# Kernel optimization log

Measured on AMD Instinct MI355X. Metric: run time of the kernel, lower is better.

Reference implementation:

```python
import jax, jax.numpy as jnp
import numpy as np
import math

WS = 8           # window size
NUM_HEADS = 8
LN_EPS = 1e-5


def window_partition(x, ws):
    # x: [B, H, W, C] -> [B*nH*nW, ws, ws, C]
    B, H, W, C = x.shape
    x = x.reshape(B, H // ws, ws, W // ws, ws, C)
    return x.transpose(0, 1, 3, 2, 4, 5).reshape(-1, ws, ws, C)


def window_reverse(w, ws, H, W):
    # w: [B*nH*nW, ws, ws, C] -> [B, H, W, C]
    B = w.shape[0] // ((H // ws) * (W // ws))
    x = w.reshape(B, H // ws, W // ws, ws, ws, -1)
    return x.transpose(0, 1, 3, 2, 4, 5).reshape(B, H, W, -1)


def layernorm(x, g, b):
    mu = jnp.mean(x, axis=-1, keepdims=True)
    var = jnp.mean(jnp.square(x - mu), axis=-1, keepdims=True)
    return (x - mu) * jax.lax.rsqrt(var + LN_EPS) * g + b


def rotation_grid(H, W, ws):
    """Vectorized rotation_process lookup table -> sampling grid [H, W, 2]=(lat,lon)."""
    nH, nW = H // ws, W // ws
    r = 1.0 / ws
    seq = -1.0 + r + 2.0 * r * jnp.arange(ws, dtype=jnp.float32)  # make_coord centers
    ch, cw = jnp.meshgrid(seq, seq, indexing='ij')
    t0 = ch.reshape(-1) / nH                       # [ws*ws] latitude template
    t1 = cw.reshape(-1) / nW                       # [ws*ws] longitude template
    beta = (2.0 * (jnp.arange(nH, dtype=jnp.float32) + 0.5) / nH - 1.0) * (math.pi / 2)  # [nH]
    th = t0 * (math.pi / 2) + math.pi / 2
    ph = t1 * math.pi
    sb, cb = jnp.sin(beta)[:, None], jnp.cos(beta)[:, None]
    st, ct = jnp.sin(th)[None, :], jnp.cos(th)[None, :]
    sp, cp = jnp.sin(ph)[None, :], jnp.cos(ph)[None, :]
    new_th = jnp.arccos(-sb * st * cp + cb * ct)                    # [nH, ws*ws]
    new_ph = jnp.arctan2(st * sp, cb * st * cp + sb * ct)
    lat = jnp.clip((new_th - math.pi / 2) / (math.pi / 2), -1.0, 1.0)
    lon = new_ph / math.pi
    shift = 2.0 * (0.5 - (jnp.arange(nW, dtype=jnp.float32) + 0.5) / nW)
    lon = lon[:, None, :] - shift[None, :, None]                    # [nH, nW, ws*ws]
    lon = jnp.where(lon > 1.0, lon - 2.0, lon)
    lon = jnp.where(lon < -1.0, lon + 2.0, lon)
    lat = jnp.broadcast_to(lat[:, None, :], lon.shape)
    g = jnp.stack([lat, lon], axis=-1).reshape(nH, nW, ws, ws, 2)
    return g.transpose(0, 2, 1, 3, 4).reshape(H, W, 2)


def grid_sample_nearest(im, grid):
    """F.grid_sample(mode='nearest', align_corners=False, padding='zeros').
    im: [B, H, W, C]; grid: [H, W, 2]=(y,x) normalized; shared across batch."""
    B, H, W, C = im.shape
    gy, gx = grid[..., 0], grid[..., 1]
    iy = jnp.round(((gy + 1.0) * H - 1.0) / 2.0).astype(jnp.int32)
    ix = jnp.round(((gx + 1.0) * W - 1.0) / 2.0).astype(jnp.int32)
    valid = (iy >= 0) & (iy < H) & (ix >= 0) & (ix < W)
    iyc = jnp.clip(iy, 0, H - 1)
    ixc = jnp.clip(ix, 0, W - 1)
    out = im[:, iyc, ixc, :]                                        # [B, H, W, C]
    return out * valid[None, :, :, None].astype(im.dtype)


def dwconv3x3(x, w, b):
    # x: [B, C, H, W], w: [C, 1, 3, 3] depthwise
    y = jax.lax.conv_general_dilated(x, w, (1, 1), 'SAME',
                                     feature_group_count=x.shape[1],
                                     dimension_numbers=('NCHW', 'OIHW', 'NCHW'))
    return y + b[None, :, None, None]


def setup_inputs() -> dict:
    key = jax.random.key(0)
    B, H, W, C, dff = 8, 64, 128, 256, 1024
    ks = jax.random.split(key, 10)
    s = 0.02
    return {
        'x': jax.random.normal(ks[0], (B, H * W, C), jnp.float32),
        'H': H, 'W': W,
        'norm1_g': jnp.ones((C,), jnp.float32),
        'norm1_b': jnp.zeros((C,), jnp.float32),
        'wq': jax.random.normal(ks[1], (C, C), jnp.float32) * s,
        'bq': jnp.zeros((C,), jnp.float32),
        'wk': jax.random.normal(ks[2], (C, C), jnp.float32) * s,
        'bk': jnp.zeros((C,), jnp.float32),
        'wv': jax.random.normal(ks[3], (C, C), jnp.float32) * s,
        'bv': jnp.zeros((C,), jnp.float32),
        'rpe_w': jax.random.normal(ks[4], (C, 1, 3, 3), jnp.float32) * s,
        'rpe_b': jnp.zeros((C,), jnp.float32),
        'proj_w': jax.random.normal(ks[5], (C, C), jnp.float32) * s,
        'proj_b': jnp.zeros((C,), jnp.float32),
        'norm2_g': jnp.ones((C,), jnp.float32),
        'norm2_b': jnp.zeros((C,), jnp.float32),
        'fc1_w': jax.random.normal(ks[6], (C, dff), jnp.float32) * s,
        'fc1_b': jnp.zeros((dff,), jnp.float32),
        'fc2_w': jax.random.normal(ks[7], (dff, C), jnp.float32) * s,
        'fc2_b': jnp.zeros((C,), jnp.float32),
    }


def reference(x, H, W, norm1_g, norm1_b, wq, bq, wk, bk, wv, bv, rpe_w, rpe_b,
              proj_w, proj_b, norm2_g, norm2_b, fc1_w, fc1_b, fc2_w, fc2_b):
    B, L, C = x.shape
    ws, nh = WS, NUM_HEADS
    hd = C // nh
    scale = hd ** (-0.5)
    N = ws * ws

    shortcut = x
    xn = layernorm(x, norm1_g, norm1_b).reshape(B, H, W, C)
    # panoramic rotation of the key features (rotation_process)
    y = grid_sample_nearest(xn, rotation_grid(H, W, ws))

    xw = window_partition(xn, ws).reshape(-1, N, C)   # [Bw, N, C]
    yw = window_partition(y, ws).reshape(-1, N, C)
    Bw = xw.shape[0]

    q = xw @ wq + bq
    # depthwise-conv positional term on window-reversed q (rpe_table)
    qimg = window_reverse(q.reshape(-1, ws, ws, C), ws, H, W).transpose(0, 3, 1, 2)  # [B,C,H,W]
    lepe = window_partition(dwconv3x3(qimg, rpe_w, rpe_b).transpose(0, 2, 3, 1), ws).reshape(-1, N, C)

    k = yw @ wk + bk
    v = xw @ wv + bv
    qh = q.reshape(Bw, N, nh, hd).transpose(0, 2, 1, 3) * scale   # [Bw,h,N,d]
    kh = k.reshape(Bw, N, nh, hd).transpose(0, 2, 1, 3)
    vh = v.reshape(Bw, N, nh, hd).transpose(0, 2, 1, 3)
    attn = jax.nn.softmax(jnp.einsum('bhnd,bhmd->bhnm', qh, kh), axis=-1)
    out = jnp.einsum('bhnm,bhmd->bhnd', attn, vh).transpose(0, 2, 1, 3).reshape(Bw, N, C)
    out = (out + lepe) @ proj_w + proj_b

    x = shortcut + window_reverse(out.reshape(-1, ws, ws, C), ws, H, W).reshape(B, L, C)
    h = layernorm(x, norm2_g, norm2_b)
    h = jax.nn.gelu(h @ fc1_w + fc1_b, approximate=False) @ fc2_w + fc2_b
    return x + h
```

## Files before the change

kernel.cpp:

```cpp
#include <hip/hip_runtime.h>

typedef __bf16 bf16;
typedef __bf16 bf16x4 __attribute__((ext_vector_type(4)));
typedef __bf16 bf16x8 __attribute__((ext_vector_type(8)));
typedef float  f32x4  __attribute__((ext_vector_type(4)));

#define HH   64
#define WW   128
#define CC   256
#define MTOK 65536
#define PI_D 3.14159265358979323846

__device__ __forceinline__ int win_row(int b, int h, int w) {
  return ((b * 8 + (h >> 3)) * 16 + (w >> 3)) * 64 + ((h & 7) << 3) + (w & 7);
}

__device__ __forceinline__ void gl_lds16(const bf16* g, bf16* l) {
  __builtin_amdgcn_global_load_lds(
      (const __attribute__((address_space(1))) unsigned int*)g,
      (__attribute__((address_space(3))) unsigned int*)l, 16, 0, 0);
}

__global__ __launch_bounds__(256) void prep_kernel(
    const float* __restrict__ wq, const float* __restrict__ wk,
    const float* __restrict__ wv, const float* __restrict__ pw,
    const float* __restrict__ f1w, const float* __restrict__ f2w,
    bf16* __restrict__ wqvT, bf16* __restrict__ wkT, bf16* __restrict__ pwT,
    bf16* __restrict__ f1T, bf16* __restrict__ f2T,
    int* __restrict__ wmap, bf16* __restrict__ zrow,
    float* __restrict__ biasqv,
    const float* __restrict__ bq, const float* __restrict__ bv) {
  const int blk = blockIdx.x;
  if (blk < 768) {
    __shared__ float tile[32][33];
    const float* src; bf16* dst; int K, N, bi;
    if (blk < 64)       { src = wq;  dst = wqvT;         K = 256;  N = 256;  bi = blk;       }
    else if (blk < 128) { src = wv;  dst = wqvT + 65536; K = 256;  N = 256;  bi = blk - 64;  }
    else if (blk < 192) { src = wk;  dst = wkT;          K = 256;  N = 256;  bi = blk - 128; }
    else if (blk < 256) { src = pw;  dst = pwT;          K = 256;  N = 256;  bi = blk - 192; }
    else if (blk < 512) { src = f1w; dst = f1T;          K = 256;  N = 1024; bi = blk - 256; }
    else                { src = f2w; dst = f2T;          K = 1024; N = 256;  bi = blk - 512; }
    const int nbk = K >> 5;
    const int bk = (bi % nbk) * 32, bn = (bi / nbk) * 32;
    const int tx = threadIdx.x & 31, ty = threadIdx.x >> 5;
#pragma unroll
    for (int r = 0; r < 4; r++)
      tile[ty + 8 * r][tx] = src[(size_t)(bk + ty + 8 * r) * N + bn + tx];
    __syncthreads();
#pragma unroll
    for (int r = 0; r < 4; r++)
      dst[(size_t)(bn + ty + 8 * r) * K + bk + tx] = (bf16)tile[tx][ty + 8 * r];
    return;
  }
  int p = (blk - 768) * 256 + threadIdx.x;
  if (p < 256) zrow[p] = (bf16)0.0f;
  if (p < 512) biasqv[p] = (p < 256) ? bq[p] : bv[p - 256];
  if (p >= HH * WW) return;
  int h = p >> 7, w = p & 127;
  int bh = h >> 3, i = h & 7, bw = w >> 3, j = w & 7;
  double seq_i = -0.875 + 0.25 * i;
  double seq_j = -0.875 + 0.25 * j;
  double t0 = seq_i / 8.0, t1 = seq_j / 16.0;
  double beta = ((bh + 0.5) / 4.0 - 1.0) * (PI_D / 2.0);
  double th = t0 * (PI_D / 2.0) + PI_D / 2.0;
  double ph = t1 * PI_D;
  double sb = sin(beta), cb = cos(beta);
  double st = sin(th),  ct = cos(th);
  double sp = sin(ph),  cp = cos(ph);
  double arg = -sb * st * cp + cb * ct;
  arg = fmin(1.0, fmax(-1.0, arg));
  double nth = acos(arg);
  double nph = atan2(st * sp, cb * st * cp + sb * ct);
  double lat = (nth - PI_D / 2.0) / (PI_D / 2.0);
  lat = fmin(1.0, fmax(-1.0, lat));
  double shift = 1.0 - (2.0 * bw + 1.0) / 16.0;
  double lon = nph / PI_D - shift;
  if (lon > 1.0) lon -= 2.0; else if (lon < -1.0) lon += 2.0;
  int iy = (int)rint(((lat + 1.0) * (double)HH - 1.0) * 0.5);
  int ix = (int)rint(((lon + 1.0) * (double)WW - 1.0) * 0.5);
  bool valid = (iy >= 0 && iy < HH && ix >= 0 && ix < WW);
  int dwr = ((h >> 3) * 16 + (w >> 3)) * 64 + ((h & 7) << 3) + (w & 7);
  int src = valid ? (((iy >> 3) * 16 + (ix >> 3)) * 64 + ((iy & 7) << 3) + (ix & 7)) : -1;
  wmap[dwr] = src;
}

__global__ __launch_bounds__(256) void ln_kernel(const float* __restrict__ x,
                                                 const float* __restrict__ g,
                                                 const float* __restrict__ bta,
                                                 bf16* __restrict__ out,
                                                 int permute) {
  int token = blockIdx.x * 4 + (threadIdx.x >> 6);
  int lane = threadIdx.x & 63;
  const float4 v = *(const float4*)(x + (size_t)token * CC + lane * 4);
  float s  = v.x + v.y + v.z + v.w;
  float ss = v.x * v.x + v.y * v.y + v.z * v.z + v.w * v.w;
#pragma unroll
  for (int o = 32; o > 0; o >>= 1) {
    s  += __shfl_xor(s, o);
    ss += __shfl_xor(ss, o);
  }
  float mu = s * (1.0f / CC);
  float var = ss * (1.0f / CC) - mu * mu;
  float rs = rsqrtf(var + 1e-5f);
  int row = token;
  if (permute) {
    int b = token >> 13, l = token & 8191;
    row = win_row(b, l >> 7, l & 127);
  }
  int c = lane * 4;
  const float4 gv = *(const float4*)(g + c);
  const float4 bv = *(const float4*)(bta + c);
  bf16x4 o4;
  o4[0] = (bf16)((v.x - mu) * rs * gv.x + bv.x);
  o4[1] = (bf16)((v.y - mu) * rs * gv.y + bv.y);
  o4[2] = (bf16)((v.z - mu) * rs * gv.z + bv.z);
  o4[3] = (bf16)((v.w - mu) * rs * gv.w + bv.w);
  *(bf16x4*)(out + (size_t)row * CC + c) = o4;
}

#define EPI_BF16 0
#define EPI_GELU 1
#define EPI_PROJ 2
#define EPI_FC2  3
#define EPI_QV   4

#define TRS 72

template <int EPI, bool GATHER>
__global__ __launch_bounds__(256) void gemm_bt(const bf16* __restrict__ A,
                                               const bf16* __restrict__ Bt,
                                               const float* __restrict__ bias,
                                               bf16* __restrict__ outB,
                                               float* __restrict__ outF,
                                               const float* __restrict__ res,
                                               const int* __restrict__ amap,
                                               const bf16* __restrict__ zrow,
                                               bf16* __restrict__ outB2,
                                               int M, int N, int K) {
  __shared__ bf16 lA[128 * 32];
  __shared__ bf16 lB[128 * 32];
  __shared__ bf16 trV[(EPI == EPI_QV) ? 4 * 64 * TRS : 4];
  const int t = threadIdx.x;
  const int wave = t >> 6, lane = t & 63;
  const int quad = lane >> 4, l16 = lane & 15;
  const int mb = blockIdx.y, nb = blockIdx.x;
  const int wm = wave >> 1, wn = wave & 1;

  f32x4 acc[4][4];
#pragma unroll
  for (int i = 0; i < 4; i++)
#pragma unroll
    for (int j = 0; j < 4; j++)
#pragma unroll
      for (int r = 0; r < 4; r++) acc[i][j][r] = 0.0f;

  const int arow = t >> 2;
  const int acol = (t & 3) << 3;
  const bf16 *gA, *gA2;
  if (GATHER) {
    int r1 = mb * 128 + arow;
    int b1 = r1 >> 13, s1 = amap[r1 & 8191];
    gA = (s1 >= 0) ? A + ((size_t)((b1 << 13) + s1)) * K + acol : zrow + acol;
    int r2 = r1 + 64;
    int b2 = r2 >> 13, s2 = amap[r2 & 8191];
    gA2 = (s2 >= 0) ? A + ((size_t)((b2 << 13) + s2)) * K + acol : zrow + acol;
  } else {
    gA = A + (size_t)(mb * 128 + arow) * K + acol;
    gA2 = gA + (size_t)64 * K;
  }
  const bf16* gB  = Bt + (size_t)(nb * 128 + arow) * K + acol;
  const bf16* gB2 = gB + (size_t)64 * K;
  bf16* lAp  = &lA[t * 8];
  bf16* lBp  = &lB[t * 8];
  bf16* lAp2 = &lA[2048 + t * 8];
  bf16* lBp2 = &lB[2048 + t * 8];

  for (int kk = 0; kk < K; kk += 32) {
    __syncthreads();
    gl_lds16(gA + kk, lAp);
    gl_lds16(gA2 + kk, lAp2);
    gl_lds16(gB + kk, lBp);
    gl_lds16(gB2 + kk, lBp2);
    __syncthreads();
    bf16x8 af[4], bfr[4];
#pragma unroll
    for (int i = 0; i < 4; i++)
      af[i] = *(const bf16x8*)&lA[(wm * 64 + i * 16 + l16) * 32 + quad * 8];
#pragma unroll
    for (int j = 0; j < 4; j++)
      bfr[j] = *(const bf16x8*)&lB[(wn * 64 + j * 16 + l16) * 32 + quad * 8];
#pragma unroll
    for (int i = 0; i < 4; i++)
#pragma unroll
      for (int j = 0; j < 4; j++)
        acc[i][j] = __builtin_amdgcn_mfma_f32_16x16x32_bf16(af[i], bfr[j], acc[i][j], 0, 0, 0);
  }

  const int m0 = mb * 128 + wm * 64;
  const int n0 = nb * 128 + wn * 64;

  if (EPI == EPI_QV && nb >= 2) {
    bf16* tw = &trV[wave * 64 * TRS];
#pragma unroll
    for (int i = 0; i < 4; i++)
#pragma unroll
      for (int j = 0; j < 4; j++) {
        const float bsv = bias[n0 + j * 16 + l16];
        bf16x4 pk;
#pragma unroll
        for (int r = 0; r < 4; r++) pk[r] = (bf16)(acc[i][j][r] + bsv);
        *(bf16x4*)&tw[(j * 16 + l16) * TRS + i * 16 + quad * 4] = pk;
      }
    const int win = mb * 2 + wm;
    const int chbase = n0 - 256;
#pragma unroll
    for (int s = 0; s < 8; s++) {
      const int ch = s * 8 + (lane >> 3);
      const int tk = (lane & 7) * 8;
      bf16x8 vv = *(const bf16x8*)&tw[ch * TRS + tk];
      *(bf16x8*)(outB2 + ((size_t)win * 256 + chbase + ch) * 64 + tk) = vv;
    }
  } else {
#pragma unroll
    for (int i = 0; i < 4; i++) {
#pragma unroll
      for (int j = 0; j < 4; j++) {
        const int col = n0 + j * 16 + l16;
        const int rowb = m0 + i * 16 + quad * 4;
        const float bsv = bias[col];
#pragma unroll
        for (int r = 0; r < 4; r++) {
          const int row = rowb + r;
          float v = acc[i][j][r] + bsv;
          if (EPI == EPI_BF16) {
            outB[(size_t)row * N + col] = (bf16)v;
          } else if (EPI == EPI_QV) {
            outB[(size_t)row * 256 + col] = (bf16)v;
          } else if (EPI == EPI_GELU) {
            float gl = 0.5f * v * (1.0f + erff(v * 0.70710678118654752f));
            outB[(size_t)row * N + col] = (bf16)gl;
          } else if (EPI == EPI_FC2) {
            size_t idx = (size_t)row * N + col;
            outF[idx] = res[idx] + v;
          } else {
            int wi = row >> 6, tt = row & 63;
            int b = wi >> 7, hb = (wi >> 4) & 7, wb = wi & 15;
            int h = hb * 8 + (tt >> 3), w = wb * 8 + (tt & 7);
            size_t idx = ((size_t)(b * 8192 + h * 128 + w)) * 256 + col;
            outF[idx] = res[idx] + v;
          }
        }
      }
    }
  }
}

__global__ __launch_bounds__(256) void lepe_kernel(const bf16* __restrict__ qb,
                                                   const float* __restrict__ rw,
                                                   const float* __restrict__ rb,
                                                   bf16* __restrict__ ao) {
  __shared__ __align__(16) bf16 hq[100 * 256];
  const int blk = blockIdx.x;
  const int b = blk >> 7, hb = (blk >> 4) & 7, wb = blk & 15;
  const int t = threadIdx.x;
  const int h0 = hb * 8 - 1, w0 = wb * 8 - 1;

  for (int idx = t; idx < 3200; idx += 256) {
    int pix = idx >> 5, ch = (idx & 31) * 8;
    int pi = pix / 10, pj = pix - pi * 10;
    int h = h0 + pi, w = w0 + pj;
    bf16x8 val;
#pragma unroll
    for (int e = 0; e < 8; e++) val[e] = (bf16)0.0f;
    if (h >= 0 && h < HH && w >= 0 && w < WW)
      val = *(const bf16x8*)(qb + (size_t)win_row(b, h, w) * 256 + ch);
    *(bf16x8*)(&hq[pix * 256 + ch]) = val;
  }
  __syncthreads();

  const int cg = t & 31, c0 = cg * 8;
  const int i = t >> 5;

  float wr[9][8];
#pragma unroll
  for (int e = 0; e < 8; e++)
#pragma unroll
    for (int tap = 0; tap < 9; tap++) wr[tap][e] = rw[(c0 + e) * 9 + tap];
  float bias[8];
  *(float4*)&bias[0] = *(const float4*)(rb + c0);
  *(float4*)&bias[4] = *(const float4*)(rb + c0 + 4);

  float cur[3][3][8];
#pragma unroll
  for (int rr = 0; rr < 3; rr++)
#pragma unroll
    for (int cc = 0; cc < 2; cc++) {
      bf16x8 v = *(const bf16x8*)(&hq[((i + rr) * 10 + cc) * 256 + c0]);
#pragma unroll
      for (int e = 0; e < 8; e++) cur[rr][cc][e] = (float)v[e];
    }

#pragma unroll
  for (int j = 0; j < 8; j++) {
    const int snew = (j + 2) % 3;
#pragma unroll
    for (int rr = 0; rr < 3; rr++) {
      bf16x8 v = *(const bf16x8*)(&hq[((i + rr) * 10 + (j + 2)) * 256 + c0]);
#pragma unroll
      for (int e = 0; e < 8; e++) cur[rr][snew][e] = (float)v[e];
    }
    float acc[8];
#pragma unroll
    for (int e = 0; e < 8; e++) acc[e] = bias[e];
#pragma unroll
    for (int rr = 0; rr < 3; rr++)
#pragma unroll
      for (int dc = 0; dc < 3; dc++) {
        const int slot = (j + dc) % 3;
        const int tap = rr * 3 + dc;
#pragma unroll
        for (int e = 0; e < 8; e++) acc[e] += cur[rr][slot][e] * wr[tap][e];
      }
    bf16x8 o;
#pragma unroll
    for (int e = 0; e < 8; e++) o[e] = (bf16)acc[e];
    *(bf16x8*)(ao + (size_t)(blk * 64 + i * 8 + j) * 256 + c0) = o;
  }
}

#define SP 74

__global__ __launch_bounds__(256) void attn_kernel(const bf16* __restrict__ qb,
                                                   const bf16* __restrict__ kb,
                                                   const bf16* __restrict__ vt,
                                                   bf16* __restrict__ ao) {
  __shared__ __align__(16) bf16 Pl[4][64 * SP];
  const int wave = threadIdx.x >> 6, lane = threadIdx.x & 63;
  const int quad = lane >> 4, l16 = lane & 15;
  const int win = blockIdx.x >> 1;
  const size_t rowbase = (size_t)win * 64;
  const int head = ((blockIdx.x & 1) << 2) + wave;
  const int hc = head * 32;
  bf16* P = Pl[wave];
  const float scale = 0.17677669529663687f;

  bf16x8 aq[4], bk4[4];
#pragma unroll
  for (int mi = 0; mi < 4; mi++)
    aq[mi] = *(const bf16x8*)(qb + (rowbase + mi * 16 + l16) * 256 + hc + quad * 8);
#pragma unroll
  for (int ni = 0; ni < 4; ni++)
    bk4[ni] = *(const bf16x8*)(kb + (rowbase + ni * 16 + l16) * 256 + hc + quad * 8);
  f32x4 sacc[4][4];
#pragma unroll
  for (int mi = 0; mi < 4; mi++)
#pragma unroll
    for (int ni = 0; ni < 4; ni++)
#pragma unroll
      for (int r = 0; r < 4; r++) sacc[mi][ni][r] = 0.0f;
#pragma unroll
  for (int mi = 0; mi < 4; mi++)
#pragma unroll
    for (int ni = 0; ni < 4; ni++)
      sacc[mi][ni] = __builtin_amdgcn_mfma_f32_16x16x32_bf16(aq[mi], bk4[ni], sacc[mi][ni], 0, 0, 0);

  bf16x8 vb2[2][2];
#pragma unroll
  for (int n0 = 0; n0 < 2; n0++)
#pragma unroll
    for (int kc = 0; kc < 2; kc++)
      vb2[n0][kc] = *(const bf16x8*)(vt + ((size_t)win * 256 + hc + n0 * 16 + l16) * 64 +
                                     kc * 32 + quad * 8);

#pragma unroll
  for (int mi = 0; mi < 4; mi++) {
#pragma unroll
    for (int r = 0; r < 4; r++) {
      float mx = -1e30f;
#pragma unroll
      for (int ni = 0; ni < 4; ni++) mx = fmaxf(mx, sacc[mi][ni][r]);
      mx = fmaxf(mx, __shfl_xor(mx, 1));
      mx = fmaxf(mx, __shfl_xor(mx, 2));
      mx = fmaxf(mx, __shfl_xor(mx, 4));
      mx = fmaxf(mx, __shfl_xor(mx, 8));
      float sm = 0.0f;
#pragma unroll
      for (int ni = 0; ni < 4; ni++) {
        float e = expf(scale * (sacc[mi][ni][r] - mx));
        sacc[mi][ni][r] = e;
        sm += e;
      }
      sm += __shfl_xor(sm, 1);
      sm += __shfl_xor(sm, 2);
      sm += __shfl_xor(sm, 4);
      sm += __shfl_xor(sm, 8);
      float inv = 1.0f / sm;
#pragma unroll
      for (int ni = 0; ni < 4; ni++) sacc[mi][ni][r] *= inv;
    }
#pragma unroll
    for (int ni = 0; ni < 4; ni++)
#pragma unroll
      for (int r = 0; r < 4; r++)
        P[(mi * 16 + quad * 4 + r) * SP + ni * 16 + l16] = (bf16)sacc[mi][ni][r];
  }

  f32x4 oacc[4][2];
#pragma unroll
  for (int mi = 0; mi < 4; mi++)
#pragma unroll
    for (int n0 = 0; n0 < 2; n0++)
#pragma unroll
      for (int r = 0; r < 4; r++) oacc[mi][n0][r] = 0.0f;
#pragma unroll
  for (int mi = 0; mi < 4; mi++)
#pragma unroll
    for (int kc = 0; kc < 2; kc++) {
      bf16x8 pf = *(const bf16x8*)&P[(mi * 16 + l16) * SP + kc * 32 + quad * 8];
#pragma unroll
      for (int n0 = 0; n0 < 2; n0++)
        oacc[mi][n0] = __builtin_amdgcn_mfma_f32_16x16x32_bf16(pf, vb2[n0][kc], oacc[mi][n0], 0, 0, 0);
    }

  bf16* Ol = P;
#pragma unroll
  for (int mi = 0; mi < 4; mi++)
#pragma unroll
    for (int n0 = 0; n0 < 2; n0++)
#pragma unroll
      for (int r = 0; r < 4; r++)
        Ol[(mi * 16 + quad * 4 + r) * 34 + n0 * 16 + l16] = (bf16)oacc[mi][n0][r];

  bf16* aop = ao + (rowbase + lane) * 256 + hc;
#pragma unroll
  for (int cc = 0; cc < 4; cc++) {
    bf16x8 ov = *(const bf16x8*)&Ol[lane * 34 + cc * 8];
    bf16x8 lp = *(const bf16x8*)(aop + cc * 8);
    bf16x8 so;
#pragma unroll
    for (int e = 0; e < 8; e++) so[e] = (bf16)((float)ov[e] + (float)lp[e]);
    *(bf16x8*)(aop + cc * 8) = so;
  }
}

extern "C" void kernel_launch(void* const* d_in, const int* in_sizes, int n_in,
                              void* d_out, int out_size, void* d_ws, size_t ws_size,
                              hipStream_t stream) {
  const float* x     = (const float*)d_in[0];
  const float* n1g   = (const float*)d_in[3];
  const float* n1b   = (const float*)d_in[4];
  const float* wq    = (const float*)d_in[5];
  const float* bq    = (const float*)d_in[6];
  const float* wk    = (const float*)d_in[7];
  const float* bk    = (const float*)d_in[8];
  const float* wv    = (const float*)d_in[9];
  const float* bv    = (const float*)d_in[10];
  const float* rpe_w = (const float*)d_in[11];
  const float* rpe_b = (const float*)d_in[12];
  const float* pw    = (const float*)d_in[13];
  const float* pb    = (const float*)d_in[14];
  const float* n2g   = (const float*)d_in[15];
  const float* n2b   = (const float*)d_in[16];
  const float* f1w   = (const float*)d_in[17];
  const float* f1b   = (const float*)d_in[18];
  const float* f2w   = (const float*)d_in[19];
  const float* f2b   = (const float*)d_in[20];
  float* out = (float*)d_out;
  char* ws = (char*)d_ws;

  const size_t A_ = 33554432ull;
  bf16* xw  = (bf16*)(ws);
  bf16* ao  = (bf16*)(ws);
  bf16* xh  = (bf16*)(ws);
  bf16* qb  = (bf16*)(ws + A_);
  bf16* vt  = (bf16*)(ws + 2 * A_);
  bf16* h1  = (bf16*)(ws + A_);
  bf16* kb  = (bf16*)d_out;
  char* wsp = ws + 3 * A_;
  bf16* wqvT = (bf16*)(wsp);
  bf16* wkT  = (bf16*)(wsp + 262144);
  bf16* pwT  = (bf16*)(wsp + 393216);
  bf16* f1T  = (bf16*)(wsp + 524288);
  bf16* f2T  = (bf16*)(wsp + 1048576);
  float* biasqv = (float*)(wsp + 1572864);
  int*   wmap   = (int*)(wsp + 1574912);
  bf16*  zrow   = (bf16*)(wsp + 1607680);

  prep_kernel<<<800, 256, 0, stream>>>(wq, wk, wv, pw, f1w, f2w,
                                       wqvT, wkT, pwT, f1T, f2T,
                                       wmap, zrow, biasqv, bq, bv);

  ln_kernel<<<MTOK / 4, 256, 0, stream>>>(x, n1g, n1b, xw, 1);

  gemm_bt<EPI_QV, false><<<dim3(4, 512), 256, 0, stream>>>(
      xw, wqvT, biasqv, qb, nullptr, nullptr, nullptr, nullptr, vt, MTOK, 512, 256);
  gemm_bt<EPI_BF16, true><<<dim3(2, 512), 256, 0, stream>>>(
      xw, wkT, bk, kb, nullptr, nullptr, wmap, zrow, nullptr, MTOK, 256, 256);

  lepe_kernel<<<1024, 256, 0, stream>>>(qb, rpe_w, rpe_b, ao);
  attn_kernel<<<2048, 256, 0, stream>>>(qb, kb, vt, ao);

  gemm_bt<EPI_PROJ, false><<<dim3(2, 512), 256, 0, stream>>>(
      ao, pwT, pb, nullptr, out, x, nullptr, nullptr, nullptr, MTOK, 256, 256);

  ln_kernel<<<MTOK / 4, 256, 0, stream>>>(out, n2g, n2b, xh, 0);

  const int CH = 32768;
  for (int c = 0; c < 2; c++) {
    gemm_bt<EPI_GELU, false><<<dim3(8, CH / 128), 256, 0, stream>>>(
        xh + (size_t)c * CH * 256, f1T, f1b, h1, nullptr, nullptr, nullptr, nullptr, nullptr,
        CH, 1024, 256);
    gemm_bt<EPI_FC2, false><<<dim3(2, CH / 128), 256, 0, stream>>>(
        h1, f2T, f2b, nullptr, out + (size_t)c * CH * 256, out + (size_t)c * CH * 256,
        nullptr, nullptr, nullptr, CH, 256, 1024);
  }
}
```

Measured before the change: 494.1 us.

## Fuse MLP fc1+GELU+fc2 into one kernel with hidden tile in LDS

Replaces the chunked fc1-GELU and fc2 GEMM launches with a single mlp_kernel. Each block computes 128 rows, loops over 128-wide hidden chunks, applies GELU into LDS and accumulates fc2 directly in registers. This removes the round-trip of the large hidden activation through global memory. It also swaps the grid axes of the remaining GEMMs so the M blocks are launched first, which may improve weight reuse in L2. Costs: only 512 blocks, high register pressure (128 fp32 accumulators plus the fc1 tile), and fc2 weights read straight from global memory without LDS staging.

```diff
diff --git a/kernel.cpp b/kernel.cpp
--- a/kernel.cpp
+++ b/kernel.cpp
@@ -19,6 +19,10 @@
   __builtin_amdgcn_global_load_lds(
       (const __attribute__((address_space(1))) unsigned int*)g,
       (__attribute__((address_space(3))) unsigned int*)l, 16, 0, 0);
+}
+
+__device__ __forceinline__ float gelu_f(float v) {
+  return 0.5f * v * (1.0f + erff(v * 0.70710678118654752f));
 }
 
 __global__ __launch_bounds__(256) void prep_kernel(
@@ -119,9 +123,7 @@
 }
 
 #define EPI_BF16 0
-#define EPI_GELU 1
 #define EPI_PROJ 2
-#define EPI_FC2  3
 #define EPI_QV   4
 
 #define TRS 72
@@ -143,7 +145,7 @@
   const int t = threadIdx.x;
   const int wave = t >> 6, lane = t & 63;
   const int quad = lane >> 4, l16 = lane & 15;
-  const int mb = blockIdx.y, nb = blockIdx.x;
+  const int mb = blockIdx.x, nb = blockIdx.y;
   const int wm = wave >> 1, wn = wave & 1;
 
   f32x4 acc[4][4];
@@ -236,12 +238,6 @@
             outB[(size_t)row * N + col] = (bf16)v;
           } else if (EPI == EPI_QV) {
             outB[(size_t)row * 256 + col] = (bf16)v;
-          } else if (EPI == EPI_GELU) {
-            float gl = 0.5f * v * (1.0f + erff(v * 0.70710678118654752f));
-            outB[(size_t)row * N + col] = (bf16)gl;
-          } else if (EPI == EPI_FC2) {
-            size_t idx = (size_t)row * N + col;
-            outF[idx] = res[idx] + v;
           } else {
             int wi = row >> 6, tt = row & 63;
             int b = wi >> 7, hb = (wi >> 4) & 7, wb = wi & 15;
@@ -253,6 +249,113 @@
       }
     }
   }
+}
+
+#define MRS 136
+
+__global__ __launch_bounds__(256) void mlp_kernel(const bf16* __restrict__ xh,
+                                                  const bf16* __restrict__ f1T,
+                                                  const float* __restrict__ f1b,
+                                                  const bf16* __restrict__ f2T,
+                                                  const float* __restrict__ f2b,
+                                                  float* __restrict__ out) {
+  __shared__ bf16 lA[128 * 32];
+  __shared__ bf16 lB[128 * 32];
+  __shared__ __align__(16) bf16 h1L[128 * MRS];
+  const int t = threadIdx.x;
+  const int wave = t >> 6, lane = t & 63;
+  const int quad = lane >> 4, l16 = lane & 15;
+  const int wm = wave >> 1, wn = wave & 1;
+  const int mb = blockIdx.x;
+  const int arow = t >> 2, acol = (t & 3) << 3;
+
+  const bf16* gA  = xh + (size_t)(mb * 128 + arow) * 256 + acol;
+  const bf16* gA2 = gA + 64 * 256;
+  bf16* lAp  = &lA[t * 8];
+  bf16* lBp  = &lB[t * 8];
+  bf16* lAp2 = &lA[2048 + t * 8];
+  bf16* lBp2 = &lB[2048 + t * 8];
+
+  f32x4 oacc[4][8];
+#pragma unroll
+  for (int i = 0; i < 4; i++)
+#pragma unroll
+    for (int j = 0; j < 8; j++)
+#pragma unroll
+      for (int r = 0; r < 4; r++) oacc[i][j][r] = 0.0f;
+
+  for (int p = 0; p < 8; p++) {
+    f32x4 acc[4][4];
+#pragma unroll
+    for (int i = 0; i < 4; i++)
+#pragma unroll
+      for (int j = 0; j < 4; j++)
+#pragma unroll
+        for (int r = 0; r < 4; r++) acc[i][j][r] = 0.0f;
+    const bf16* gB  = f1T + (size_t)(p * 128 + arow) * 256 + acol;
+    const bf16* gB2 = gB + 64 * 256;
+    for (int kk = 0; kk < 256; kk += 32) {
+      __syncthreads();
+      gl_lds16(gA + kk, lAp);
+      gl_lds16(gA2 + kk, lAp2);
+      gl_lds16(gB + kk, lBp);
+      gl_lds16(gB2 + kk, lBp2);
+      __syncthreads();
+      bf16x8 af[4], bfr[4];
+#pragma unroll
+      for (int i = 0; i < 4; i++)
+        af[i] = *(const bf16x8*)&lA[(wm * 64 + i * 16 + l16) * 32 + quad * 8];
+#pragma unroll
+      for (int j = 0; j < 4; j++)
+        bfr[j] = *(const bf16x8*)&lB[(wn * 64 + j * 16 + l16) * 32 + quad * 8];
+#pragma unroll
+      for (int i = 0; i < 4; i++)
+#pragma unroll
+        for (int j = 0; j < 4; j++)
+          acc[i][j] = __builtin_amdgcn_mfma_f32_16x16x32_bf16(af[i], bfr[j], acc[i][j], 0, 0, 0);
+    }
+#pragma unroll
+    for (int i = 0; i < 4; i++)
+#pragma unroll
+      for (int j = 0; j < 4; j++) {
+        const int hcol = wn * 64 + j * 16 + l16;
+        const float bsv = f1b[p * 128 + hcol];
+        const int hrowb = wm * 64 + i * 16 + quad * 4;
+#pragma unroll
+        for (int r = 0; r < 4; r++)
+          h1L[(hrowb + r) * MRS + hcol] = (bf16)gelu_f(acc[i][j][r] + bsv);
+      }
+    __syncthreads();
+#pragma unroll
+    for (int kc = 0; kc < 4; kc++) {
+      bf16x8 af[4];
+#pragma unroll
+      for (int i = 0; i < 4; i++)
+        af[i] = *(const bf16x8*)&h1L[(wm * 64 + i * 16 + l16) * MRS + kc * 32 + quad * 8];
+#pragma unroll
+      for (int j = 0; j < 8; j++) {
+        bf16x8 bfr = *(const bf16x8*)(f2T + (size_t)(wn * 128 + j * 16 + l16) * 1024 +
+                                      p * 128 + kc * 32 + quad * 8);
+#pragma unroll
+        for (int i = 0; i < 4; i++)
+          oacc[i][j] = __builtin_amdgcn_mfma_f32_16x16x32_bf16(af[i], bfr, oacc[i][j], 0, 0, 0);
+      }
+    }
+  }
+
+#pragma unroll
+  for (int i = 0; i < 4; i++)
+#pragma unroll
+    for (int j = 0; j < 8; j++) {
+      const int col = wn * 128 + j * 16 + l16;
+      const float bsv = f2b[col];
+      const int rowb = mb * 128 + wm * 64 + i * 16 + quad * 4;
+#pragma unroll
+      for (int r = 0; r < 4; r++) {
+        size_t idx = (size_t)(rowb + r) * 256 + col;
+        out[idx] = out[idx] + oacc[i][j][r] + bsv;
+      }
+    }
 }
 
 __global__ __launch_bounds__(256) void lepe_kernel(const bf16* __restrict__ qb,
@@ -474,7 +577,6 @@
   bf16* xh  = (bf16*)(ws);
   bf16* qb  = (bf16*)(ws + A_);
   bf16* vt  = (bf16*)(ws + 2 * A_);
-  bf16* h1  = (bf16*)(ws + A_);
   bf16* kb  = (bf16*)d_out;
   char* wsp = ws + 3 * A_;
   bf16* wqvT = (bf16*)(wsp);
@@ -492,26 +594,18 @@
 
   ln_kernel<<<MTOK / 4, 256, 0, stream>>>(x, n1g, n1b, xw, 1);
 
-  gemm_bt<EPI_QV, false><<<dim3(4, 512), 256, 0, stream>>>(
+  gemm_bt<EPI_QV, false><<<dim3(512, 4), 256, 0, stream>>>(
       xw, wqvT, biasqv, qb, nullptr, nullptr, nullptr, nullptr, vt, MTOK, 512, 256);
-  gemm_bt<EPI_BF16, true><<<dim3(2, 512), 256, 0, stream>>>(
+  gemm_bt<EPI_BF16, true><<<dim3(512, 2), 256, 0, stream>>>(
       xw, wkT, bk, kb, nullptr, nullptr, wmap, zrow, nullptr, MTOK, 256, 256);
 
   lepe_kernel<<<1024, 256, 0, stream>>>(qb, rpe_w, rpe_b, ao);
   attn_kernel<<<2048, 256, 0, stream>>>(qb, kb, vt, ao);
 
-  gemm_bt<EPI_PROJ, false><<<dim3(2, 512), 256, 0, stream>>>(
+  gemm_bt<EPI_PROJ, false><<<dim3(512, 2), 256, 0, stream>>>(
       ao, pwT, pb, nullptr, out, x, nullptr, nullptr, nullptr, MTOK, 256, 256);
 
   ln_kernel<<<MTOK / 4, 256, 0, stream>>>(out, n2g, n2b, xh, 0);
 
-  const int CH = 32768;
-  for (int c = 0; c < 2; c++) {
-    gemm_bt<EPI_GELU, false><<<dim3(8, CH / 128), 256, 0, stream>>>(
-        xh + (size_t)c * CH * 256, f1T, f1b, h1, nullptr, nullptr, nullptr, nullptr, nullptr,
-        CH, 1024, 256);
-    gemm_bt<EPI_FC2, false><<<dim3(2, CH / 128), 256, 0, stream>>>(
-        h1, f2T, f2b, nullptr, out + (size_t)c * CH * 256, out + (size_t)c * CH * 256,
-        nullptr, nullptr, nullptr, CH, 256, 1024);
-  }
-}
+  mlp_kernel<<<512, 256, 0, stream>>>(xh, f1T, f1b, f2T, f2b, out);
+}
```

Measured after the change: 583.1 us. +18.0%, slower.
